# Kernel optimization log

Measured on AMD Instinct MI355X. Metric: run time of the kernel, lower is better.

The kernel has to match this reference:

```python
import jax, jax.numpy as jnp
import numpy as np

N_BINS = 15


def setup_inputs() -> dict:
    key = jax.random.key(0)
    k1, k2 = jax.random.split(key)
    N, C = 2097152, 50
    logits = jax.random.normal(k1, (N, C), dtype=jnp.float32)
    labels = jax.random.randint(k2, (N,), 0, C, dtype=jnp.int64)
    return {"logits": logits, "labels": labels}


def reference(logits, labels):
    n = logits.shape[0]
    probs = jax.nn.softmax(logits, axis=1)
    confidences = jnp.max(probs, axis=1)                 # [N]
    predictions = jnp.argmax(probs, axis=1)              # [N]
    accuracies = (predictions == labels).astype(jnp.float32)

    # bin i covers (i/n_bins, (i+1)/n_bins]; searchsorted(left) on the upper
    # boundaries gives the first upper >= conf, matching conf.gt(lo)*conf.le(hi)
    uppers = jnp.linspace(0.0, 1.0, N_BINS + 1)[1:]
    bin_id = jnp.clip(jnp.searchsorted(uppers, confidences, side="left"), 0, N_BINS - 1)

    ones = jnp.ones_like(confidences)
    counts = jax.ops.segment_sum(ones, bin_id, num_segments=N_BINS)
    sum_acc = jax.ops.segment_sum(accuracies, bin_id, num_segments=N_BINS)
    sum_conf = jax.ops.segment_sum(confidences, bin_id, num_segments=N_BINS)

    prop_in_bin = counts / n
    nonempty = counts > 0
    denom = jnp.maximum(counts, 1.0)
    avg_acc = sum_acc / denom
    avg_conf = sum_conf / denom

    gap = avg_conf - avg_acc
    bin_over_confidence = jnp.where(nonempty, gap * prop_in_bin, 0.0)   # [n_bins]
    ece = jnp.sum(jnp.where(nonempty, jnp.abs(gap) * prop_in_bin, 0.0)).reshape(1)
    return (ece, bin_over_confidence, prop_in_bin)
```

## Files before the change

kernel.cpp:

```cpp
#include <hip/hip_runtime.h>
#include <math.h>

#define N_BINS 15
#define C 50
#define RPB 256
#define PAD 51


__global__ __launch_bounds__(RPB) void ece_accum(
    const float* __restrict__ logits,
    const int*   __restrict__ labels,
    unsigned int* __restrict__ ws_cnt,
    unsigned int* __restrict__ ws_acc,
    float*        __restrict__ ws_conf,
    int n_rows)
{
    __shared__ float tile[RPB * PAD];
    __shared__ unsigned int s_cnt[N_BINS];
    __shared__ unsigned int s_acc[N_BINS];
    __shared__ float        s_conf[N_BINS];

    const int tid = threadIdx.x;
    if (tid < N_BINS) { s_cnt[tid] = 0u; s_acc[tid] = 0u; s_conf[tid] = 0.0f; }

    const long long row0 = (long long)blockIdx.x * RPB;
    const float* __restrict__ src = logits + row0 * C;
    const long long rem_rows = (long long)n_rows - row0;
    const int rows_here = (rem_rows >= RPB) ? RPB : (int)(rem_rows > 0 ? rem_rows : 0);

    if (rows_here == RPB) {
        const float4* __restrict__ src4 = (const float4*)src;
        for (int i = tid; i < (RPB * C) / 4; i += RPB) {
            float4 v = src4[i];
            int base = 4 * i;
            int r    = base / C;
            int rem  = base - r * C;
            int addr = base + r;
            if (rem <= C - 4) {
                tile[addr]     = v.x;
                tile[addr + 1] = v.y;
                tile[addr + 2] = v.z;
                tile[addr + 3] = v.w;
            } else {
                float e[4] = {v.x, v.y, v.z, v.w};
                #pragma unroll
                for (int j = 0; j < 4; ++j) {
                    int ee = base + j;
                    tile[ee + ee / C] = e[j];
                }
            }
        }
    } else {
        int tot = rows_here * C;
        for (int i = tid; i < tot; i += RPB) tile[i + i / C] = src[i];
    }
    __syncthreads();

    const long long row = row0 + tid;
    if (row < (long long)n_rows && tid < rows_here) {
        const float* __restrict__ r = &tile[tid * PAD];
        float vals[C];
        float vmax = -INFINITY;
        int   amax = 0;
        #pragma unroll
        for (int k = 0; k < C; ++k) {
            float v = r[k];
            vals[k] = v;
            if (v > vmax) { vmax = v; amax = k; }
        }
        float sum = 0.0f;
        #pragma unroll
        for (int k = 0; k < C; ++k) sum += __expf(vals[k] - vmax);
        float conf = 1.0f / sum;

        int bin = (int)ceilf(conf * 15.0f) - 1;
        bin = bin < 0 ? 0 : (bin > N_BINS - 1 ? N_BINS - 1 : bin);

        int correct = (amax == labels[row]) ? 1 : 0;

        atomicAdd(&s_cnt[bin], 1u);
        if (correct) atomicAdd(&s_acc[bin], 1u);
        atomicAdd(&s_conf[bin], conf);
    }
    __syncthreads();

    if (tid < N_BINS && s_cnt[tid] != 0u) {
        atomicAdd(&ws_cnt[tid], s_cnt[tid]);
        atomicAdd(&ws_acc[tid], s_acc[tid]);
        atomicAdd(&ws_conf[tid], s_conf[tid]);
    }
}

__global__ __launch_bounds__(64) void ece_final(
    const unsigned int* __restrict__ ws_cnt,
    const unsigned int* __restrict__ ws_acc,
    const float*        __restrict__ ws_conf,
    float* __restrict__ out, float inv_n)
{
    int i = threadIdx.x;
    float v = 0.0f;
    if (i < N_BINS) {
        float cnt      = (float)ws_cnt[i];
        float prop     = cnt * inv_n;
        float denom    = fmaxf(cnt, 1.0f);
        float avg_acc  = (float)ws_acc[i] / denom;
        float avg_conf = ws_conf[i] / denom;
        float gap      = avg_conf - avg_acc;
        bool  nonempty = cnt > 0.0f;
        out[1 + i]  = nonempty ? gap * prop : 0.0f;
        out[16 + i] = prop;
        v = nonempty ? fabsf(gap) * prop : 0.0f;
    }
    v += __shfl_down(v, 8, 64);
    v += __shfl_down(v, 4, 64);
    v += __shfl_down(v, 2, 64);
    v += __shfl_down(v, 1, 64);
    if (i == 0) out[0] = v;
}

extern "C" void kernel_launch(void* const* d_in, const int* in_sizes, int n_in,
                              void* d_out, int out_size, void* d_ws, size_t ws_size,
                              hipStream_t stream)
{
    const float* logits = (const float*)d_in[0];
    const int*   labels = (const int*)d_in[1];
    const int n_rows = in_sizes[1];

    unsigned int* ws_cnt  = (unsigned int*)d_ws;
    unsigned int* ws_acc  = ws_cnt + N_BINS;
    float*        ws_conf = (float*)(ws_acc + N_BINS);

    hipMemsetAsync(d_ws, 0, 3 * N_BINS * sizeof(float), stream);

    int grid = (n_rows + RPB - 1) / RPB;
    ece_accum<<<grid, RPB, 0, stream>>>(logits, labels, ws_cnt, ws_acc, ws_conf, n_rows);
    ece_final<<<1, 64, 0, stream>>>(ws_cnt, ws_acc, ws_conf, (float*)d_out,
                                    1.0f / (float)n_rows);
}
```

Measured before the change: 682.1 us.

## Use persistent per-wave tiles with direct global-to-LDS loads

Replaces the one-block-per-256-rows scheme with a fixed grid of 768 blocks in which each wave loops over 64-row tiles. Each tile is staged into its own LDS region through global_load_lds, which skips the register round trip and the padded scatter. Per-block bin atomics now happen once after many tiles instead of once per 256 rows. The cost is no overlap between a wave's load and its compute, and unpadded rows read as float2 from LDS, which may cause bank conflicts.

```diff
diff --git a/kernel.cpp b/kernel.cpp
--- a/kernel.cpp
+++ b/kernel.cpp
@@ -3,11 +3,20 @@
 
 #define N_BINS 15
 #define C 50
-#define RPB 256
-#define PAD 51
+#define ROWS_PER_TILE 64
+#define TILE_FLOATS (ROWS_PER_TILE * C)
+#define WAVES_PER_BLOCK 4
+#define BLOCK (WAVES_PER_BLOCK * 64)
+#define GRID 768
 
 
-__global__ __launch_bounds__(RPB) void ece_accum(
+__device__ __forceinline__ void load_lds16(const float* g, float* l) {
+    __builtin_amdgcn_global_load_lds(
+        (const __attribute__((address_space(1))) unsigned int*)g,
+        (__attribute__((address_space(3))) unsigned int*)l, 16, 0, 0);
+}
+
+__global__ __launch_bounds__(BLOCK) void ece_accum(
     const float* __restrict__ logits,
     const int*   __restrict__ labels,
     unsigned int* __restrict__ ws_cnt,
@@ -15,59 +24,53 @@
     float*        __restrict__ ws_conf,
     int n_rows)
 {
-    __shared__ float tile[RPB * PAD];
+    __shared__ float tiles[WAVES_PER_BLOCK * TILE_FLOATS];
     __shared__ unsigned int s_cnt[N_BINS];
     __shared__ unsigned int s_acc[N_BINS];
     __shared__ float        s_conf[N_BINS];
 
     const int tid = threadIdx.x;
     if (tid < N_BINS) { s_cnt[tid] = 0u; s_acc[tid] = 0u; s_conf[tid] = 0.0f; }
-
-    const long long row0 = (long long)blockIdx.x * RPB;
-    const float* __restrict__ src = logits + row0 * C;
-    const long long rem_rows = (long long)n_rows - row0;
-    const int rows_here = (rem_rows >= RPB) ? RPB : (int)(rem_rows > 0 ? rem_rows : 0);
-
-    if (rows_here == RPB) {
-        const float4* __restrict__ src4 = (const float4*)src;
-        for (int i = tid; i < (RPB * C) / 4; i += RPB) {
-            float4 v = src4[i];
-            int base = 4 * i;
-            int r    = base / C;
-            int rem  = base - r * C;
-            int addr = base + r;
-            if (rem <= C - 4) {
-                tile[addr]     = v.x;
-                tile[addr + 1] = v.y;
-                tile[addr + 2] = v.z;
-                tile[addr + 3] = v.w;
-            } else {
-                float e[4] = {v.x, v.y, v.z, v.w};
-                #pragma unroll
-                for (int j = 0; j < 4; ++j) {
-                    int ee = base + j;
-                    tile[ee + ee / C] = e[j];
-                }
-            }
-        }
-    } else {
-        int tot = rows_here * C;
-        for (int i = tid; i < tot; i += RPB) tile[i + i / C] = src[i];
-    }
     __syncthreads();
 
-    const long long row = row0 + tid;
-    if (row < (long long)n_rows && tid < rows_here) {
-        const float* __restrict__ r = &tile[tid * PAD];
+    const int wave = tid >> 6;
+    const int lane = tid & 63;
+    float* __restrict__ wtile = &tiles[wave * TILE_FLOATS];
+
+    const int n_tiles  = n_rows / ROWS_PER_TILE;
+    const int gwave    = blockIdx.x * WAVES_PER_BLOCK + wave;
+    const int n_gwaves = GRID * WAVES_PER_BLOCK;
+
+    for (int t = gwave; t < n_tiles; t += n_gwaves) {
+        const float* __restrict__ src = logits + (size_t)t * TILE_FLOATS;
+
+        asm volatile("s_waitcnt lgkmcnt(0)" ::: "memory");
+
+        #pragma unroll
+        for (int j = 0; j < 12; ++j)
+            load_lds16(src + (j * 64 + lane) * 4, wtile + j * 256);
+        if (lane < 32)
+            load_lds16(src + (12 * 64 + lane) * 4, wtile + 12 * 256);
+
+        int label = labels[t * ROWS_PER_TILE + lane];
+
+        asm volatile("s_waitcnt vmcnt(0)" ::: "memory");
+
+        const float2* __restrict__ r2 = (const float2*)(wtile + lane * C);
         float vals[C];
-        float vmax = -INFINITY;
+        #pragma unroll
+        for (int k = 0; k < C / 2; ++k) {
+            float2 p = r2[k];
+            vals[2 * k]     = p.x;
+            vals[2 * k + 1] = p.y;
+        }
+
+        float vmax = vals[0];
         int   amax = 0;
         #pragma unroll
-        for (int k = 0; k < C; ++k) {
-            float v = r[k];
-            vals[k] = v;
-            if (v > vmax) { vmax = v; amax = k; }
-        }
+        for (int k = 1; k < C; ++k)
+            if (vals[k] > vmax) { vmax = vals[k]; amax = k; }
+
         float sum = 0.0f;
         #pragma unroll
         for (int k = 0; k < C; ++k) sum += __expf(vals[k] - vmax);
@@ -76,17 +79,35 @@
         int bin = (int)ceilf(conf * 15.0f) - 1;
         bin = bin < 0 ? 0 : (bin > N_BINS - 1 ? N_BINS - 1 : bin);
 
-        int correct = (amax == labels[row]) ? 1 : 0;
-
         atomicAdd(&s_cnt[bin], 1u);
-        if (correct) atomicAdd(&s_acc[bin], 1u);
+        if (amax == label) atomicAdd(&s_acc[bin], 1u);
         atomicAdd(&s_conf[bin], conf);
     }
+
+    const int rem_start = n_tiles * ROWS_PER_TILE;
+    const int rem = n_rows - rem_start;
+    if (blockIdx.x == 0 && tid < rem) {
+        const float* __restrict__ r = logits + (size_t)(rem_start + tid) * C;
+        float vmax = r[0];
+        int   amax = 0;
+        for (int k = 1; k < C; ++k) {
+            float v = r[k];
+            if (v > vmax) { vmax = v; amax = k; }
+        }
+        float sum = 0.0f;
+        for (int k = 0; k < C; ++k) sum += __expf(r[k] - vmax);
+        float conf = 1.0f / sum;
+        int bin = (int)ceilf(conf * 15.0f) - 1;
+        bin = bin < 0 ? 0 : (bin > N_BINS - 1 ? N_BINS - 1 : bin);
+        atomicAdd(&s_cnt[bin], 1u);
+        if (amax == labels[rem_start + tid]) atomicAdd(&s_acc[bin], 1u);
+        atomicAdd(&s_conf[bin], conf);
+    }
+
     __syncthreads();
-
     if (tid < N_BINS && s_cnt[tid] != 0u) {
-        atomicAdd(&ws_cnt[tid], s_cnt[tid]);
-        atomicAdd(&ws_acc[tid], s_acc[tid]);
+        atomicAdd(&ws_cnt[tid],  s_cnt[tid]);
+        atomicAdd(&ws_acc[tid],  s_acc[tid]);
         atomicAdd(&ws_conf[tid], s_conf[tid]);
     }
 }
@@ -132,8 +153,7 @@
 
     hipMemsetAsync(d_ws, 0, 3 * N_BINS * sizeof(float), stream);
 
-    int grid = (n_rows + RPB - 1) / RPB;
-    ece_accum<<<grid, RPB, 0, stream>>>(logits, labels, ws_cnt, ws_acc, ws_conf, n_rows);
+    ece_accum<<<GRID, BLOCK, 0, stream>>>(logits, labels, ws_cnt, ws_acc, ws_conf, n_rows);
     ece_final<<<1, 64, 0, stream>>>(ws_cnt, ws_acc, ws_conf, (float*)d_out,
                                     1.0f / (float)n_rows);
 }
```

Measured after the change: 553.3 us. 18.9% less time.
